# Performance work log

Measured on AMD Instinct MI355X. Metric: run time of the kernel, lower is better.

The kernel has to match this reference:

```python
import jax, jax.numpy as jnp
import numpy as np

HEADS = 8


def setup_inputs() -> dict:
    key = jax.random.key(0)
    k1, k2, k3 = jax.random.split(key, 3)
    B, H, W, C = 4, 64, 64, 1024
    x1 = jax.random.normal(k1, (B, H, W, C), jnp.float32)
    x2 = jax.random.normal(k2, (B, H, W, C), jnp.float32)
    w_proj = jax.random.normal(k3, (2 * C, C), jnp.float32) * 0.02  # 1x1 conv weight [out,in]
    b_proj = jnp.zeros((2 * C,), jnp.float32)
    gamma = jnp.ones((2 * C,), jnp.float32)   # LayerNorm weight
    beta = jnp.zeros((2 * C,), jnp.float32)   # LayerNorm bias
    return {"x1": x1, "x2": x2, "w_proj": w_proj, "b_proj": b_proj, "gamma": gamma, "beta": beta}


def reference(x1, x2, w_proj, b_proj, gamma, beta):
    B, H, W, C = x1.shape
    N = H * W
    h = HEADS
    c = C // h  # per-head channels (key == value channels here)
    # [B,H,W,C] -> [B,C,N] -> [B,h,c,N]; concat over heads in torch is head-major in C,
    # so this reshape matches torch.cat(..., dim=1).reshape(B, C, H, W).
    value = x1.reshape(B, N, C).transpose(0, 2, 1).reshape(B, h, c, N)
    kq = x2.reshape(B, N, C).transpose(0, 2, 1).reshape(B, h, c, N)
    key = jax.nn.softmax(kq, axis=-1)   # softmax over tokens N (torch dim=2)
    query = jax.nn.softmax(kq, axis=2)  # softmax over per-head channels (torch dim=1)
    # attended = query @ (value^T @ key)^T == (query @ key^T) @ value  (exact reassociation,
    # avoids materializing the [N,N] context the per-head torch loop builds)
    S = jnp.einsum('bhin,bhjn->bhij', query, key)    # [B,h,c,c]
    att = jnppad = jnp.einsum('bhij,bhjn->bhin', S, value)  # [B,h,c,N]
    agg = att.reshape(B, C, H, W)
    # 1x1 conv C -> 2C, then permute to channels-last
    y = jnp.einsum('oc,bchw->bhwo', w_proj, agg) + b_proj  # [B,H,W,2C]
    # LayerNorm over last dim, eps=1e-5 (torch default)
    mu = jnp.mean(y, axis=-1, keepdims=True)
    var = jnp.var(y, axis=-1, keepdims=True)
    return (y - mu) / jnp.sqrt(var + 1e-5) * gamma + beta
```

## Files before the change

kernel.cpp:

```cpp
#include <hip/hip_runtime.h>
#include <stdint.h>

#define AS1 __attribute__((address_space(1)))
#define AS3 __attribute__((address_space(3)))

using bf16x8_t = __attribute__((ext_vector_type(8))) __bf16;
using f32x4_t  = __attribute__((ext_vector_type(4))) float;

__device__ __forceinline__ uint16_t f2bf(float f) {
    union { float f; uint32_t u; } v; v.f = f;
    return (uint16_t)((v.u + 0x7fffu + ((v.u >> 16) & 1u)) >> 16);
}
__device__ __forceinline__ float bf2f(uint16_t h) {
    union { uint32_t u; float f; } v; v.u = ((uint32_t)h) << 16;
    return v.f;
}

__global__ __launch_bounds__(256) void k_convert(const float* __restrict__ x,
                                                 uint16_t* __restrict__ o, int n4) {
    int i = blockIdx.x * 256 + threadIdx.x;
    int stride = gridDim.x * 256;
    for (; i < n4; i += stride) {
        float4 v = ((const float4*)x)[i];
        ushort4 u;
        u.x = f2bf(v.x); u.y = f2bf(v.y); u.z = f2bf(v.z); u.w = f2bf(v.w);
        ((ushort4*)o)[i] = u;
    }
}

__global__ __launch_bounds__(256) void k_sF(const float* __restrict__ x2,
                                            float* __restrict__ spart,
                                            float* __restrict__ colsum) {
    int bx = blockIdx.x;
    int bh = bx & 31, ns = bx >> 5;
    int b = bh >> 3, h = bh & 7;
    __shared__ uint32_t F[128 * 64];
    __shared__ float cs[128];
    int t = threadIdx.x;
    int g = t & 15, rp = t >> 4;
    int w = t >> 6, l = t & 63;
    int c15 = l & 15, kg = l >> 4;
    if (t < 128) cs[t] = 0.f;
    f32x4_t acc[8][2];
    #pragma unroll
    for (int it = 0; it < 8; ++it) {
        acc[it][0] = (f32x4_t){0.f, 0.f, 0.f, 0.f};
        acc[it][1] = (f32x4_t){0.f, 0.f, 0.f, 0.f};
    }
    float csl[8] = {0.f, 0.f, 0.f, 0.f, 0.f, 0.f, 0.f, 0.f};
    const float* xb = x2 + ((size_t)(b * 4096 + ns * 256)) * 1024 + h * 128 + g * 8;
    int swz = g & 7;
    for (int half = 0; half < 2; ++half) {
        if (half) __syncthreads();
        #pragma unroll
        for (int it = 0; it < 4; ++it) {
            int np = rp + it * 16;
            int n0 = half * 128 + np * 2;
            const float* p0 = xb + (size_t)n0 * 1024;
            float4 a0 = ((const float4*)p0)[0];
            float4 a1 = ((const float4*)p0)[1];
            float4 b0 = ((const float4*)(p0 + 1024))[0];
            float4 b1 = ((const float4*)(p0 + 1024))[1];
            float e0[8], e1[8];
            e0[0] = __expf(a0.x); e0[1] = __expf(a0.y); e0[2] = __expf(a0.z); e0[3] = __expf(a0.w);
            e0[4] = __expf(a1.x); e0[5] = __expf(a1.y); e0[6] = __expf(a1.z); e0[7] = __expf(a1.w);
            e1[0] = __expf(b0.x); e1[1] = __expf(b0.y); e1[2] = __expf(b0.z); e1[3] = __expf(b0.w);
            e1[4] = __expf(b1.x); e1[5] = __expf(b1.y); e1[6] = __expf(b1.z); e1[7] = __expf(b1.w);
            float s0 = ((e0[0]+e0[1])+(e0[2]+e0[3])) + ((e0[4]+e0[5])+(e0[6]+e0[7]));
            float s1 = ((e1[0]+e1[1])+(e1[2]+e1[3])) + ((e1[4]+e1[5])+(e1[6]+e1[7]));
            #pragma unroll
            for (int m2 = 1; m2 < 16; m2 <<= 1) {
                s0 += __shfl_xor(s0, m2);
                s1 += __shfl_xor(s1, m2);
            }
            float r0 = rsqrtf(s0), r1 = rsqrtf(s1);
            int blk = it * 4 + (rp >> 2);
            uint32_t* Fw = &F[g * 512 + ((blk ^ swz) << 2) + (rp & 3)];
            #pragma unroll
            for (int m = 0; m < 8; ++m) {
                Fw[m * 64] = (uint32_t)f2bf(e0[m] * r0) | ((uint32_t)f2bf(e1[m] * r1) << 16);
                csl[m] += e0[m] + e1[m];
            }
        }
        __syncthreads();
        #pragma unroll
        for (int kk2 = 0; kk2 < 4; ++kk2) {
            bf16x8_t Bf[2];
            #pragma unroll
            for (int jt = 0; jt < 2; ++jt) {
                int c = w * 32 + jt * 16 + c15;
                Bf[jt] = *(const bf16x8_t*)&F[c * 64 + (((kk2 * 4 + kg) ^ ((c >> 3) & 7)) << 2)];
            }
            #pragma unroll
            for (int it = 0; it < 8; ++it) {
                int c = it * 16 + c15;
                bf16x8_t Af = *(const bf16x8_t*)&F[c * 64 + (((kk2 * 4 + kg) ^ ((c >> 3) & 7)) << 2)];
                acc[it][0] = __builtin_amdgcn_mfma_f32_16x16x32_bf16(Af, Bf[0], acc[it][0], 0, 0, 0);
                acc[it][1] = __builtin_amdgcn_mfma_f32_16x16x32_bf16(Af, Bf[1], acc[it][1], 0, 0, 0);
            }
        }
    }
    #pragma unroll
    for (int m = 0; m < 8; ++m) {
        csl[m] += __shfl_xor(csl[m], 16);
        csl[m] += __shfl_xor(csl[m], 32);
    }
    if ((t & 48) == 0) {
        #pragma unroll
        for (int m = 0; m < 8; ++m) atomicAdd(&cs[g * 8 + m], csl[m]);
    }
    __syncthreads();
    if (t < 128) atomicAdd(&colsum[b * 1024 + h * 128 + t], cs[t]);
    float* sp = spart + ((size_t)(ns * 32 + bh)) * 16384;
    #pragma unroll
    for (int it = 0; it < 8; ++it)
        #pragma unroll
        for (int jt = 0; jt < 2; ++jt)
            #pragma unroll
            for (int q = 0; q < 4; ++q)
                sp[(it * 16 + kg * 4 + q) * 128 + w * 32 + jt * 16 + c15] = acc[it][jt][q];
}

__global__ __launch_bounds__(256) void k_sred(const float* __restrict__ spart,
                                              const float* __restrict__ colsum,
                                              uint16_t* __restrict__ SbfT) {
    int bx = blockIdx.x;
    int bh = bx >> 3, ic = bx & 7;
    int b = bh >> 3, h = bh & 7;
    __shared__ float T[128 * 17];
    int t = threadIdx.x;
    int il = t >> 4, g = t & 15;
    int i = ic * 16 + il;
    const float* sp = spart + (size_t)bh * 16384 + (size_t)i * 128 + g * 8;
    float v[8] = {0.f, 0.f, 0.f, 0.f, 0.f, 0.f, 0.f, 0.f};
    #pragma unroll
    for (int ns = 0; ns < 16; ++ns) {
        float4 u0 = ((const float4*)(sp + (size_t)ns * 524288))[0];
        float4 u1 = ((const float4*)(sp + (size_t)ns * 524288))[1];
        v[0] += u0.x; v[1] += u0.y; v[2] += u0.z; v[3] += u0.w;
        v[4] += u1.x; v[5] += u1.y; v[6] += u1.z; v[7] += u1.w;
    }
    const float* cp = colsum + b * 1024 + h * 128 + g * 8;
    float4 c0 = ((const float4*)cp)[0];
    float4 c1 = ((const float4*)cp)[1];
    T[(g * 8 + 0) * 17 + il] = v[0] / c0.x;
    T[(g * 8 + 1) * 17 + il] = v[1] / c0.y;
    T[(g * 8 + 2) * 17 + il] = v[2] / c0.z;
    T[(g * 8 + 3) * 17 + il] = v[3] / c0.w;
    T[(g * 8 + 4) * 17 + il] = v[4] / c1.x;
    T[(g * 8 + 5) * 17 + il] = v[5] / c1.y;
    T[(g * 8 + 6) * 17 + il] = v[6] / c1.z;
    T[(g * 8 + 7) * 17 + il] = v[7] / c1.w;
    __syncthreads();
    int j = t >> 1, ih = t & 1;
    const float* tp = &T[j * 17 + ih * 8];
    uint4 o;
    o.x = (uint32_t)f2bf(tp[0]) | ((uint32_t)f2bf(tp[1]) << 16);
    o.y = (uint32_t)f2bf(tp[2]) | ((uint32_t)f2bf(tp[3]) << 16);
    o.z = (uint32_t)f2bf(tp[4]) | ((uint32_t)f2bf(tp[5]) << 16);
    o.w = (uint32_t)f2bf(tp[6]) | ((uint32_t)f2bf(tp[7]) << 16);
    *(uint4*)(SbfT + (size_t)bh * 16384 + (size_t)j * 128 + ic * 16 + ih * 8) = o;
}

__global__ __launch_bounds__(256) void k_fold(const uint16_t* __restrict__ Wbf,
                                              const uint16_t* __restrict__ SbfT,
                                              uint16_t* __restrict__ Wb) {
    int bx = blockIdx.x;
    int ot = bx & 15, h = (bx >> 4) & 7, b = bx >> 7;
    int bh = b * 8 + h;
    int t = threadIdx.x;
    int w = t >> 6, l = t & 63;
    int c15 = l & 15, kg = l >> 4;
    f32x4_t acc[2][8];
    #pragma unroll
    for (int it2 = 0; it2 < 2; ++it2)
        #pragma unroll
        for (int jt = 0; jt < 8; ++jt)
            acc[it2][jt] = (f32x4_t){0.f, 0.f, 0.f, 0.f};
    const uint16_t* Abase = Wbf + (size_t)(ot * 128 + w * 32 + c15) * 1024 + h * 128 + kg * 8;
    const uint16_t* Bbase = SbfT + (size_t)bh * 16384 + (size_t)c15 * 128 + kg * 8;
    #pragma unroll
    for (int kk2 = 0; kk2 < 4; ++kk2) {
        bf16x8_t Af0 = *(const bf16x8_t*)(Abase + kk2 * 32);
        bf16x8_t Af1 = *(const bf16x8_t*)(Abase + 16 * 1024 + kk2 * 32);
        bf16x8_t Bf[8];
        #pragma unroll
        for (int jt = 0; jt < 8; ++jt)
            Bf[jt] = *(const bf16x8_t*)(Bbase + (size_t)jt * 16 * 128 + kk2 * 32);
        #pragma unroll
        for (int jt = 0; jt < 8; ++jt) {
            acc[0][jt] = __builtin_amdgcn_mfma_f32_16x16x32_bf16(Af0, Bf[jt], acc[0][jt], 0, 0, 0);
            acc[1][jt] = __builtin_amdgcn_mfma_f32_16x16x32_bf16(Af1, Bf[jt], acc[1][jt], 0, 0, 0);
        }
    }
    #pragma unroll
    for (int it2 = 0; it2 < 2; ++it2)
        #pragma unroll
        for (int jt = 0; jt < 8; ++jt)
            #pragma unroll
            for (int q = 0; q < 4; ++q) {
                int o = ot * 128 + w * 32 + it2 * 16 + kg * 4 + q;
                int j = jt * 16 + c15;
                Wb[((size_t)b * 2048 + o) * 1024 + h * 128 + j] = f2bf(acc[it2][jt][q]);
            }
}

__global__ __launch_bounds__(256) void k_gemm(const uint16_t* __restrict__ A,
                                              const uint16_t* __restrict__ Bw,
                                              uint16_t* __restrict__ Y) {
    int bx = blockIdx.x;
    bx = ((bx & 7) << 8) | (bx >> 3);
    int ct = bx & 15, rt = (bx >> 4) & 31, b = bx >> 9;
    __shared__ uint16_t As[128 * 32];
    __shared__ uint16_t Bs[128 * 32];
    int t = threadIdx.x;
    int w = t >> 6, l = t & 63;
    int wr = w >> 1, wc = w & 1;
    const uint16_t* Ab = A + (size_t)(b * 4096 + rt * 128) * 1024;
    const uint16_t* Bb = Bw + (size_t)b * 2048 * 1024 + (size_t)(ct * 128) * 1024;
    f32x4_t acc[4][4];
    #pragma unroll
    for (int m = 0; m < 4; ++m)
        #pragma unroll
        for (int n = 0; n < 4; ++n)
            acc[m][n] = (f32x4_t){0.f, 0.f, 0.f, 0.f};
    int srow = t >> 2;
    int scol = (t & 3) * 8;
    uint16_t* AsW = &As[w * 512];
    uint16_t* BsW = &Bs[w * 512];
    int lr = l & 15, lk = (l >> 4) * 8;
    for (int kt = 0; kt < 32; ++kt) {
        const uint16_t* Ak = Ab + (size_t)srow * 1024 + kt * 32 + scol;
        const uint16_t* Bk = Bb + (size_t)srow * 1024 + kt * 32 + scol;
        __builtin_amdgcn_global_load_lds((const AS1 void*)Ak, (AS3 void*)AsW, 16, 0, 0);
        __builtin_amdgcn_global_load_lds((const AS1 void*)(Ak + 64 * 1024), (AS3 void*)(AsW + 2048), 16, 0, 0);
        __builtin_amdgcn_global_load_lds((const AS1 void*)Bk, (AS3 void*)BsW, 16, 0, 0);
        __builtin_amdgcn_global_load_lds((const AS1 void*)(Bk + 64 * 1024), (AS3 void*)(BsW + 2048), 16, 0, 0);
        __syncthreads();
        bf16x8_t af[4], bfv[4];
        #pragma unroll
        for (int m = 0; m < 4; ++m)
            af[m] = *(const bf16x8_t*)&As[(wr * 64 + m * 16 + lr) * 32 + lk];
        #pragma unroll
        for (int n = 0; n < 4; ++n)
            bfv[n] = *(const bf16x8_t*)&Bs[(wc * 64 + n * 16 + lr) * 32 + lk];
        #pragma unroll
        for (int m = 0; m < 4; ++m)
            #pragma unroll
            for (int n = 0; n < 4; ++n)
                acc[m][n] = __builtin_amdgcn_mfma_f32_16x16x32_bf16(af[m], bfv[n], acc[m][n], 0, 0, 0);
        __syncthreads();
    }
    int lq = l >> 4;
    size_t rowb = (size_t)b * 4096 + rt * 128 + wr * 64;
    int colb = ct * 128 + wc * 64;
    #pragma unroll
    for (int m = 0; m < 4; ++m)
        #pragma unroll
        for (int n = 0; n < 4; ++n)
            #pragma unroll
            for (int q = 0; q < 4; ++q) {
                size_t row = rowb + m * 16 + lq * 4 + q;
                int col = colb + n * 16 + lr;
                Y[row * 2048 + col] = f2bf(acc[m][n][q]);
            }
}

__global__ __launch_bounds__(256) void k_ln(const uint16_t* __restrict__ Yb,
                                            const float* __restrict__ bproj,
                                            const float* __restrict__ gamma,
                                            const float* __restrict__ beta,
                                            float* __restrict__ out) {
    int row = blockIdx.x;
    int t = threadIdx.x;
    const uint16_t* yp = Yb + (size_t)row * 2048 + t * 8;
    ushort4 u0 = ((const ushort4*)yp)[0];
    ushort4 u1 = ((const ushort4*)yp)[1];
    float4 bp0 = ((const float4*)(bproj + t * 8))[0];
    float4 bp1 = ((const float4*)(bproj + t * 8))[1];
    float v[8];
    v[0] = bf2f(u0.x) + bp0.x; v[1] = bf2f(u0.y) + bp0.y;
    v[2] = bf2f(u0.z) + bp0.z; v[3] = bf2f(u0.w) + bp0.w;
    v[4] = bf2f(u1.x) + bp1.x; v[5] = bf2f(u1.y) + bp1.y;
    v[6] = bf2f(u1.z) + bp1.z; v[7] = bf2f(u1.w) + bp1.w;
    float s = 0.f, q = 0.f;
    #pragma unroll
    for (int k = 0; k < 8; ++k) { s += v[k]; q += v[k] * v[k]; }
    #pragma unroll
    for (int m = 1; m < 64; m <<= 1) {
        s += __shfl_xor(s, m);
        q += __shfl_xor(q, m);
    }
    __shared__ float rs[4], rq[4];
    int w = t >> 6, l = t & 63;
    if (l == 0) { rs[w] = s; rq[w] = q; }
    __syncthreads();
    s = rs[0] + rs[1] + rs[2] + rs[3];
    q = rq[0] + rq[1] + rq[2] + rq[3];
    float mu = s * (1.0f / 2048.0f);
    float var = q * (1.0f / 2048.0f) - mu * mu;
    float rstd = rsqrtf(var + 1e-5f);
    float4 g0 = ((const float4*)(gamma + t * 8))[0];
    float4 g1 = ((const float4*)(gamma + t * 8))[1];
    float4 be0 = ((const float4*)(beta + t * 8))[0];
    float4 be1 = ((const float4*)(beta + t * 8))[1];
    float* op = out + (size_t)row * 2048 + t * 8;
    float4 o0, o1;
    o0.x = (v[0] - mu) * rstd * g0.x + be0.x;
    o0.y = (v[1] - mu) * rstd * g0.y + be0.y;
    o0.z = (v[2] - mu) * rstd * g0.z + be0.z;
    o0.w = (v[3] - mu) * rstd * g0.w + be0.w;
    o1.x = (v[4] - mu) * rstd * g1.x + be1.x;
    o1.y = (v[5] - mu) * rstd * g1.y + be1.y;
    o1.z = (v[6] - mu) * rstd * g1.z + be1.z;
    o1.w = (v[7] - mu) * rstd * g1.w + be1.w;
    ((float4*)op)[0] = o0;
    ((float4*)op)[1] = o1;
}

extern "C" void kernel_launch(void* const* d_in, const int* in_sizes, int n_in,
                              void* d_out, int out_size, void* d_ws, size_t ws_size,
                              hipStream_t stream) {
    const float* x1    = (const float*)d_in[0];
    const float* x2    = (const float*)d_in[1];
    const float* wproj = (const float*)d_in[2];
    const float* bproj = (const float*)d_in[3];
    const float* gamma = (const float*)d_in[4];
    const float* beta  = (const float*)d_in[5];
    float* out = (float*)d_out;

    char* ws = (char*)d_ws;
    uint16_t* x1bf   = (uint16_t*)(ws);
    uint16_t* Wbf    = (uint16_t*)(ws + 33554432);
    uint16_t* Wb     = (uint16_t*)(ws + 37748736);
    uint16_t* Y      = (uint16_t*)(ws + 54525952);
    float*    spart  = (float*)   (ws + 54525952);
    uint16_t* SbfT   = (uint16_t*)(ws + 121634816);
    float*    colsum = (float*)   (ws + 122683392);

    hipMemsetAsync(colsum, 0, 4096 * sizeof(float), stream);
    k_convert<<<2048, 256, 0, stream>>>(x1, x1bf, 4194304);
    k_convert<<<512, 256, 0, stream>>>(wproj, Wbf, 524288);
    k_sF<<<512, 256, 0, stream>>>(x2, spart, colsum);
    k_sred<<<256, 256, 0, stream>>>(spart, colsum, SbfT);
    k_fold<<<512, 256, 0, stream>>>(Wbf, SbfT, Wb);
    k_gemm<<<2048, 256, 0, stream>>>(x1bf, Wb, Y);
    k_ln<<<16384, 256, 0, stream>>>(Y, bproj, gamma, beta, out);
}
```

Baseline: 375.3 us.

## Rewrite GEMM with 256x256 tiles, triple-buffered async LDS loads and swizzle

```diff
diff --git a/kernel.cpp b/kernel.cpp
--- a/kernel.cpp
+++ b/kernel.cpp
@@ -205,57 +205,100 @@
             }
 }
 
-__global__ __launch_bounds__(256) void k_gemm(const uint16_t* __restrict__ A,
-                                              const uint16_t* __restrict__ Bw,
-                                              uint16_t* __restrict__ Y) {
+__global__ __launch_bounds__(512, 2) void k_gemm(const uint16_t* __restrict__ A,
+                                                 const uint16_t* __restrict__ Bw,
+                                                 uint16_t* __restrict__ Y) {
+    __shared__ uint16_t LA[3][8192];
+    __shared__ uint16_t LB[3][8192];
     int bx = blockIdx.x;
-    bx = ((bx & 7) << 8) | (bx >> 3);
-    int ct = bx & 15, rt = (bx >> 4) & 31, b = bx >> 9;
-    __shared__ uint16_t As[128 * 32];
-    __shared__ uint16_t Bs[128 * 32];
+    int swz = ((bx & 7) << 6) | (bx >> 3);
+    int ct = swz & 7, rt = swz >> 3;
+    int b = rt >> 4;
     int t = threadIdx.x;
     int w = t >> 6, l = t & 63;
-    int wr = w >> 1, wc = w & 1;
-    const uint16_t* Ab = A + (size_t)(b * 4096 + rt * 128) * 1024;
-    const uint16_t* Bb = Bw + (size_t)b * 2048 * 1024 + (size_t)(ct * 128) * 1024;
-    f32x4_t acc[4][4];
-    #pragma unroll
-    for (int m = 0; m < 4; ++m)
+    int wr = w >> 2, wc = w & 3;
+    int lr = l & 15, kg = l >> 4;
+    int sg = (kg ^ (lr & 3)) << 3;
+
+    const uint16_t* Ablk = A + (size_t)rt * 256 * 1024;
+    const uint16_t* Bblk = Bw + (size_t)b * 2048 * 1024 + (size_t)ct * 256 * 1024;
+
+    const uint16_t* aSrc[2];
+    const uint16_t* bSrc[2];
+    int ldso[2];
+    #pragma unroll
+    for (int rnd = 0; rnd < 2; ++rnd) {
+        int idx = rnd * 512 + t;
+        int r = idx >> 2, g = idx & 3;
+        int gc = ((g ^ (r & 3)) << 3);
+        aSrc[rnd] = Ablk + (size_t)r * 1024 + gc;
+        bSrc[rnd] = Bblk + (size_t)r * 1024 + gc;
+        ldso[rnd] = (rnd * 512 + w * 64) * 8;
+    }
+
+    f32x4_t acc[8][4];
+    #pragma unroll
+    for (int m = 0; m < 8; ++m)
         #pragma unroll
         for (int n = 0; n < 4; ++n)
             acc[m][n] = (f32x4_t){0.f, 0.f, 0.f, 0.f};
-    int srow = t >> 2;
-    int scol = (t & 3) * 8;
-    uint16_t* AsW = &As[w * 512];
-    uint16_t* BsW = &Bs[w * 512];
-    int lr = l & 15, lk = (l >> 4) * 8;
+
+    uint16_t *pa0 = &LA[0][0], *pa1 = &LA[1][0], *pa2 = &LA[2][0];
+    uint16_t *pb0 = &LB[0][0], *pb1 = &LB[1][0], *pb2 = &LB[2][0];
+
+    #pragma unroll
+    for (int rnd = 0; rnd < 2; ++rnd) {
+        __builtin_amdgcn_global_load_lds((const AS1 void*)(aSrc[rnd]), (AS3 void*)(pa0 + ldso[rnd]), 16, 0, 0);
+        __builtin_amdgcn_global_load_lds((const AS1 void*)(bSrc[rnd]), (AS3 void*)(pb0 + ldso[rnd]), 16, 0, 0);
+    }
+    #pragma unroll
+    for (int rnd = 0; rnd < 2; ++rnd) {
+        __builtin_amdgcn_global_load_lds((const AS1 void*)(aSrc[rnd] + 32), (AS3 void*)(pa1 + ldso[rnd]), 16, 0, 0);
+        __builtin_amdgcn_global_load_lds((const AS1 void*)(bSrc[rnd] + 32), (AS3 void*)(pb1 + ldso[rnd]), 16, 0, 0);
+    }
+
     for (int kt = 0; kt < 32; ++kt) {
-        const uint16_t* Ak = Ab + (size_t)srow * 1024 + kt * 32 + scol;
-        const uint16_t* Bk = Bb + (size_t)srow * 1024 + kt * 32 + scol;
-        __builtin_amdgcn_global_load_lds((const AS1 void*)Ak, (AS3 void*)AsW, 16, 0, 0);
-        __builtin_amdgcn_global_load_lds((const AS1 void*)(Ak + 64 * 1024), (AS3 void*)(AsW + 2048), 16, 0, 0);
-        __builtin_amdgcn_global_load_lds((const AS1 void*)Bk, (AS3 void*)BsW, 16, 0, 0);
-        __builtin_amdgcn_global_load_lds((const AS1 void*)(Bk + 64 * 1024), (AS3 void*)(BsW + 2048), 16, 0, 0);
-        __syncthreads();
-        bf16x8_t af[4], bfv[4];
-        #pragma unroll
-        for (int m = 0; m < 4; ++m)
-            af[m] = *(const bf16x8_t*)&As[(wr * 64 + m * 16 + lr) * 32 + lk];
+        if (kt < 30) {
+            int kc = (kt + 2) * 32;
+            #pragma unroll
+            for (int rnd = 0; rnd < 2; ++rnd) {
+                __builtin_amdgcn_global_load_lds((const AS1 void*)(aSrc[rnd] + kc), (AS3 void*)(pa2 + ldso[rnd]), 16, 0, 0);
+                __builtin_amdgcn_global_load_lds((const AS1 void*)(bSrc[rnd] + kc), (AS3 void*)(pb2 + ldso[rnd]), 16, 0, 0);
+            }
+            asm volatile("s_waitcnt vmcnt(8)" ::: "memory");
+        } else if (kt == 30) {
+            asm volatile("s_waitcnt vmcnt(4)" ::: "memory");
+        } else {
+            asm volatile("s_waitcnt vmcnt(0)" ::: "memory");
+        }
+        asm volatile("s_barrier" ::: "memory");
+
+        bf16x8_t af[8], bfr[4];
+        #pragma unroll
+        for (int m = 0; m < 8; ++m)
+            af[m] = *(const bf16x8_t*)(pa0 + (wr * 128 + m * 16 + lr) * 32 + sg);
         #pragma unroll
         for (int n = 0; n < 4; ++n)
-            bfv[n] = *(const bf16x8_t*)&Bs[(wc * 64 + n * 16 + lr) * 32 + lk];
-        #pragma unroll
-        for (int m = 0; m < 4; ++m)
+            bfr[n] = *(const bf16x8_t*)(pb0 + (wc * 64 + n * 16 + lr) * 32 + sg);
+        __builtin_amdgcn_s_setprio(1);
+        #pragma unroll
+        for (int m = 0; m < 8; ++m)
             #pragma unroll
             for (int n = 0; n < 4; ++n)
-                acc[m][n] = __builtin_amdgcn_mfma_f32_16x16x32_bf16(af[m], bfv[n], acc[m][n], 0, 0, 0);
-        __syncthreads();
-    }
+                acc[m][n] = __builtin_amdgcn_mfma_f32_16x16x32_bf16(af[m], bfr[n], acc[m][n], 0, 0, 0);
+        __builtin_amdgcn_s_setprio(0);
+        asm volatile("s_barrier" ::: "memory");
+
+        uint16_t* tmp;
+        tmp = pa0; pa0 = pa1; pa1 = pa2; pa2 = tmp;
+        tmp = pb0; pb0 = pb1; pb1 = pb2; pb2 = tmp;
+    }
+
     int lq = l >> 4;
-    size_t rowb = (size_t)b * 4096 + rt * 128 + wr * 64;
-    int colb = ct * 128 + wc * 64;
-    #pragma unroll
-    for (int m = 0; m < 4; ++m)
+    size_t rowb = (size_t)rt * 256 + wr * 128;
+    int colb = ct * 256 + wc * 64;
+    #pragma unroll
+    for (int m = 0; m < 8; ++m)
         #pragma unroll
         for (int n = 0; n < 4; ++n)
             #pragma unroll
@@ -344,6 +387,6 @@
     k_sF<<<512, 256, 0, stream>>>(x2, spart, colsum);
     k_sred<<<256, 256, 0, stream>>>(spart, colsum, SbfT);
     k_fold<<<512, 256, 0, stream>>>(Wbf, SbfT, Wb);
-    k_gemm<<<2048, 256, 0, stream>>>(x1bf, Wb, Y);
+    k_gemm<<<512, 512, 0, stream>>>(x1bf, Wb, Y);
     k_ln<<<16384, 256, 0, stream>>>(Y, bproj, gamma, beta, out);
 }
```

Result: no change. 381.2 us (+1.6%).
